# Kernel tuning notes

Hardware: AMD Instinct MI355X
Metric: run time of the kernel (lower is better)

The kernel has to match this reference:

```python
import jax, jax.numpy as jnp
import numpy as np

B, D, N, H = 4, 256, 2048, 4
HEAD_DIM = D // H


def conv1x1(W, b, x):
    # Conv1d(kernel_size=1): [B, Cin, N] -> [B, Cout, N]
    return jnp.einsum('oi,bin->bon', W, x) + b[None, :, None]


def setup_inputs() -> dict:
    key = jax.random.key(0)
    ks = jax.random.split(key, 8)
    s = 0.05
    return {
        'x': jax.random.normal(ks[0], (B, D, N), jnp.float32),
        'source': jax.random.normal(ks[1], (B, D, N), jnp.float32),
        'edge': jax.random.uniform(ks[2], (B, N, N), jnp.float32),
        'Wq': jax.random.normal(ks[3], (D, D), jnp.float32) * s,
        'bq': jnp.zeros((D,), jnp.float32),
        'Wk': jax.random.normal(ks[4], (D, D), jnp.float32) * s,
        'bk': jnp.zeros((D,), jnp.float32),
        'Wv': jax.random.normal(ks[5], (D, D), jnp.float32) * s,
        'bv': jnp.zeros((D,), jnp.float32),
        'Wm': jax.random.normal(ks[6], (D, D), jnp.float32) * s,
        'bm': jnp.zeros((D,), jnp.float32),
        'W1': jax.random.normal(ks[7], (2 * D, 2 * D), jnp.float32) * s,
        'b1': jnp.zeros((2 * D,), jnp.float32),
        'W2': jax.random.normal(jax.random.fold_in(key, 99), (D, 2 * D), jnp.float32) * s,
        'b2': jnp.zeros((D,), jnp.float32),
    }


def reference(x, source, edge, Wq, bq, Wk, bk, Wv, bv, Wm, bm, W1, b1, W2, b2):
    b = x.shape[0]
    # projections, then split channels D -> (head_dim, H), matching torch .view
    q = conv1x1(Wq, bq, x).reshape(b, HEAD_DIM, H, -1)       # [B, d, H, N]
    k = conv1x1(Wk, bk, source).reshape(b, HEAD_DIM, H, -1)  # [B, d, H, M]
    v = conv1x1(Wv, bv, source).reshape(b, HEAD_DIM, H, -1)
    scores = jnp.einsum('bdhn,bdhm->bhnm', q, k) / jnp.sqrt(jnp.float32(HEAD_DIM))
    prob = jax.nn.softmax(scores, axis=-1) * edge[:, None, :, :]  # edge-weighted probs
    msg = jnp.einsum('bhnm,bdhm->bdhn', prob, v).reshape(b, D, -1)
    message = conv1x1(Wm, bm, msg)                           # merge heads
    h = jnp.concatenate([x, message], axis=1)                # [B, 2D, N]
    h = jax.nn.relu(conv1x1(W1, b1, h))
    return conv1x1(W2, b2, h)                                # [B, D, N]
```

## Files before the change

### kernel.cpp

```cpp
#include <hip/hip_runtime.h>
#include <math.h>

#define B_ 4
#define D_ 256
#define N_ 2048
#define H_ 4

typedef __attribute__((ext_vector_type(8))) __bf16 bf16x8;
typedef __attribute__((ext_vector_type(4))) __bf16 bf16x4;
typedef __attribute__((ext_vector_type(4))) float f32x4;

template <typename OutT>
__device__ __forceinline__ void conv_tile(
    const float* __restrict__ in1, int C1,
    const float* __restrict__ in2, int C2,
    const float* __restrict__ Wt, const float* __restrict__ bias,
    OutT* __restrict__ out, int Cout, int K, int RELU, float oscale,
    int b, int o0, int n0, __bf16 (*sXT)[72])
{
    const int t = threadIdx.x;
    const int w  = t >> 6;
    const int g  = (t >> 4) & 3;
    const int c16 = t & 15;
    const int d_ld = t & 63;
    const int xcol = (t >> 6) * 16;

    f32x4 acc[4];
#pragma unroll
    for (int i = 0; i < 4; ++i) acc[i] = (f32x4){0.f, 0.f, 0.f, 0.f};

    float4 xreg[4];
    float4 wreg[4];
    const int ow = o0 + 16 * w + c16;

    auto LOADX = [&](int ks) {
        const int ch = ks + d_ld;
        const float* src = (ch < C1)
            ? in1 + ((size_t)b * C1 + ch) * N_ + n0 + xcol
            : in2 + ((size_t)b * C2 + (ch - C1)) * N_ + n0 + xcol;
#pragma unroll
        for (int j = 0; j < 4; ++j) xreg[j] = *(const float4*)&src[4 * j];
    };
    auto LOADW = [&](int ks) {
        wreg[0] = *(const float4*)&Wt[(size_t)ow * K + ks + 8 * g];
        wreg[1] = *(const float4*)&Wt[(size_t)ow * K + ks + 8 * g + 4];
        wreg[2] = *(const float4*)&Wt[(size_t)ow * K + ks + 32 + 8 * g];
        wreg[3] = *(const float4*)&Wt[(size_t)ow * K + ks + 32 + 8 * g + 4];
    };
    auto WRITEXT = [&](int buf) {
        __bf16 (*sx)[72] = sXT + (size_t)buf * 64;
#pragma unroll
        for (int j = 0; j < 4; ++j) {
            const float xf[4] = {xreg[j].x, xreg[j].y, xreg[j].z, xreg[j].w};
#pragma unroll
            for (int i = 0; i < 4; ++i)
                sx[xcol + 4 * j + i][d_ld] = (__bf16)xf[i];
        }
    };

    LOADX(0);
    LOADW(0);
    WRITEXT(0);
    __syncthreads();

    const int nsteps = K >> 6;
    for (int s = 0; s < nsteps; ++s) {
        const int cur = s & 1;
        const int ks = s << 6;
        if (s + 1 < nsteps) LOADX(ks + 64);

        bf16x8 af[2];
#pragma unroll
        for (int kc = 0; kc < 2; ++kc) {
            const float* w0 = (const float*)&wreg[2 * kc];
            const float* w1 = (const float*)&wreg[2 * kc + 1];
#pragma unroll
            for (int i = 0; i < 4; ++i) {
                af[kc][i]     = (__bf16)w0[i];
                af[kc][i + 4] = (__bf16)w1[i];
            }
        }
        if (s + 1 < nsteps) LOADW(ks + 64);

        __bf16 (*sx)[72] = sXT + (size_t)cur * 64;
#pragma unroll
        for (int kc = 0; kc < 2; ++kc)
#pragma unroll
            for (int nsub = 0; nsub < 4; ++nsub) {
                const bf16x8 bfr = *(const bf16x8*)&sx[16 * nsub + c16][32 * kc + 8 * g];
                acc[nsub] = __builtin_amdgcn_mfma_f32_16x16x32_bf16(af[kc], bfr, acc[nsub], 0, 0, 0);
            }

        if (s + 1 < nsteps) WRITEXT(cur ^ 1);
        __syncthreads();
    }

#pragma unroll
    for (int nsub = 0; nsub < 4; ++nsub)
#pragma unroll
        for (int r = 0; r < 4; ++r) {
            const int o = o0 + 16 * w + 4 * g + r;
            float v = acc[nsub][r] + bias[o];
            if (RELU) v = fmaxf(v, 0.f);
            v *= oscale;
            out[((size_t)b * Cout + o) * N_ + n0 + 16 * nsub + c16] = (OutT)v;
        }
}

template <int RELU>
__global__ __launch_bounds__(256) void mfma_conv_kernel(
    const float* __restrict__ in1, int C1,
    const float* __restrict__ in2, int C2,
    const float* __restrict__ W, const float* __restrict__ bias,
    float* __restrict__ out, int Cout, int K)
{
    __shared__ __bf16 sXT[2 * 64][72];
    conv_tile<float>(in1, C1, in2, C2, W, bias, out, Cout, K, RELU, 1.0f,
                     blockIdx.z, blockIdx.y * 64, blockIdx.x * 64, sXT);
}

__global__ __launch_bounds__(256) void qkv_conv_kernel(
    const float* __restrict__ x, const float* __restrict__ source,
    const float* __restrict__ Wq, const float* __restrict__ bq,
    const float* __restrict__ Wk, const float* __restrict__ bk,
    const float* __restrict__ Wv, const float* __restrict__ bv,
    __bf16* __restrict__ Qo, __bf16* __restrict__ Ko, __bf16* __restrict__ Vo)
{
    __shared__ __bf16 sXT[2 * 64][72];
    const int sel = blockIdx.y >> 2;
    const int o0  = (blockIdx.y & 3) * 64;
    const float* in = (sel == 0) ? x : source;
    const float* W  = (sel == 0) ? Wq : (sel == 1) ? Wk : Wv;
    const float* bs = (sel == 0) ? bq : (sel == 1) ? bk : bv;
    __bf16* out     = (sel == 0) ? Qo : (sel == 1) ? Ko : Vo;
    const float sc  = (sel == 1) ? 0.125f : 1.0f;
    conv_tile<__bf16>(in, D_, nullptr, 0, W, bs, out, D_, D_, 0, sc,
                      blockIdx.z, o0, blockIdx.x * 64, sXT);
}

template <int NSPLIT>
__global__ __launch_bounds__(256, 4) void attn_kernel(
    const __bf16* __restrict__ Qg, const __bf16* __restrict__ Kg,
    const __bf16* __restrict__ Vg, const float* __restrict__ edge,
    __bf16* __restrict__ OP, float* __restrict__ ML)
{
    const int nt    = blockIdx.x;
    const int n0    = nt * 64;
    const int split = blockIdx.y % NSPLIT;
    const int h     = blockIdx.y / NSPLIT;
    const int b     = blockIdx.z;
    const int t  = threadIdx.x;
    const int w  = t >> 6;
    const int g  = (t >> 4) & 3;
    const int c16 = t & 15;

    const int MT   = 32 / NSPLIT;
    const int m_lo = split * (N_ / NSPLIT);
    const int pid  = ((b * H_ + h) * NSPLIT + split) * 32 + nt;

    __shared__ __bf16 sKT[64][72];
    __shared__ __bf16 sP [64][72];

    bf16x8 qf[2];
#pragma unroll
    for (int kc = 0; kc < 2; ++kc)
#pragma unroll
        for (int e = 0; e < 8; ++e) {
            const int d = 32 * kc + 8 * g + e;
            qf[kc][e] = Qg[((size_t)b * D_ + d * H_ + h) * N_ + n0 + 16 * w + c16];
        }

    f32x4 acc[4];
#pragma unroll
    for (int i = 0; i < 4; ++i) acc[i] = (f32x4){0.f, 0.f, 0.f, 0.f};
    float Lr[4];
#pragma unroll
    for (int r = 0; r < 4; ++r) Lr[r] = 0.f;

    const int d_ld = t & 63;
    const int wv   = t >> 6;
    const size_t kbase = ((size_t)b * D_ + d_ld * H_ + h) * N_ + m_lo + wv * 16;
    const size_t vrow  = ((size_t)b * D_ + (16 * w + c16) * H_ + h) * N_ + m_lo;
    const size_t ebase = ((size_t)b * N_ + n0 + 16 * w + 4 * g) * N_ + m_lo + c16;

    bf16x8 kreg[2];
    bf16x8 vreg[2];
    float  ereg[4][4];

    auto LOADK = [&](int m0) {
        kreg[0] = *(const bf16x8*)&Kg[kbase + m0];
        kreg[1] = *(const bf16x8*)&Kg[kbase + m0 + 8];
    };
    auto LOADV = [&](int m0) {
        vreg[0] = *(const bf16x8*)&Vg[vrow + m0 + 8 * g];
        vreg[1] = *(const bf16x8*)&Vg[vrow + m0 + 32 + 8 * g];
    };
    auto LOADE = [&](int m0) {
#pragma unroll
        for (int r = 0; r < 4; ++r)
#pragma unroll
            for (int ms = 0; ms < 4; ++ms)
                ereg[r][ms] = edge[ebase + (size_t)r * N_ + m0 + 16 * ms];
    };
    auto WRITEKT = [&]() {
        const __bf16* kp = (const __bf16*)kreg;
#pragma unroll
        for (int i = 0; i < 16; ++i)
            sKT[wv * 16 + i][d_ld] = kp[i];
    };

    LOADK(0);
    LOADV(0);
    LOADE(0);
    WRITEKT();
    __syncthreads();

    for (int mt = 0; mt < MT; ++mt) {
        const int m0n = (mt < MT - 1 ? mt + 1 : mt) * 64;

        const bf16x8 af0 = vreg[0], af1 = vreg[1];
        LOADK(m0n);
        LOADV(m0n);

        f32x4 sfrag[4];
#pragma unroll
        for (int msub = 0; msub < 4; ++msub) {
            f32x4 s = (f32x4){0.f, 0.f, 0.f, 0.f};
#pragma unroll
            for (int kc = 0; kc < 2; ++kc) {
                const bf16x8 bfr = *(const bf16x8*)&sKT[16 * msub + c16][32 * kc + 8 * g];
                s = __builtin_amdgcn_mfma_f32_16x16x32_bf16(qf[kc], bfr, s, 0, 0, 0);
            }
            sfrag[msub] = s;
        }

#pragma unroll
        for (int msub = 0; msub < 4; ++msub) {
#pragma unroll
            for (int r = 0; r < 4; ++r) {
                const int nloc = 16 * w + 4 * g + r;
                const float p = __expf(sfrag[msub][r]);
                Lr[r] += p;
                sP[nloc][16 * msub + c16] = (__bf16)(p * ereg[r][msub]);
            }
        }
        LOADE(m0n);

        __syncthreads();

#pragma unroll
        for (int nsub = 0; nsub < 4; ++nsub) {
            const bf16x8 b0 = *(const bf16x8*)&sP[16 * nsub + c16][8 * g];
            acc[nsub] = __builtin_amdgcn_mfma_f32_16x16x32_bf16(af0, b0, acc[nsub], 0, 0, 0);
            const bf16x8 b1 = *(const bf16x8*)&sP[16 * nsub + c16][32 + 8 * g];
            acc[nsub] = __builtin_amdgcn_mfma_f32_16x16x32_bf16(af1, b1, acc[nsub], 0, 0, 0);
        }
        WRITEKT();

        __syncthreads();
    }

#pragma unroll
    for (int mask = 1; mask < 16; mask <<= 1)
#pragma unroll
        for (int r = 0; r < 4; ++r) Lr[r] += __shfl_xor(Lr[r], mask);
    if (c16 == 0) {
#pragma unroll
        for (int r = 0; r < 4; ++r) {
            const int nloc = 16 * w + 4 * g + r;
            ML[(size_t)pid * 128 + nloc]      = 0.0f;
            ML[(size_t)pid * 128 + 64 + nloc] = Lr[r];
        }
    }
#pragma unroll
    for (int nsub = 0; nsub < 4; ++nsub)
#pragma unroll
        for (int r = 0; r < 4; ++r) {
            const int dd = 16 * w + 4 * g + r;
            OP[(size_t)pid * 4096 + dd * 64 + 16 * nsub + c16] = (__bf16)acc[nsub][r];
        }
}

template <int NSPLIT>
__global__ __launch_bounds__(256) void combine_kernel(
    const __bf16* __restrict__ OP, const float* __restrict__ ML,
    float* __restrict__ msg)
{
    const int nt = blockIdx.x;
    const int h  = blockIdx.y;
    const int b  = blockIdx.z;
    const int t  = threadIdx.x;
    const int d  = t & 63;
    const int seg = t >> 6;
    const int pid0 = ((b * H_ + h) * NSPLIT) * 32 + nt;

    __shared__ float sM[NSPLIT][64], sL[NSPLIT][64];
    if (t < NSPLIT * 64) {
        const int s = t >> 6, n = t & 63;
        sM[s][n] = ML[(size_t)(pid0 + s * 32) * 128 + n];
        sL[s][n] = ML[(size_t)(pid0 + s * 32) * 128 + 64 + n];
    }
    __syncthreads();

#pragma unroll
    for (int q = 0; q < 4; ++q) {
        const int c0 = seg * 16 + q * 4;
        float o[4] = {0.f, 0.f, 0.f, 0.f};
        float wgt[NSPLIT][4];
#pragma unroll
        for (int j = 0; j < 4; ++j) {
            float mx = -3.0e38f;
            for (int s = 0; s < NSPLIT; ++s) mx = fmaxf(mx, sM[s][c0 + j]);
            float den = 0.f;
            for (int s = 0; s < NSPLIT; ++s) {
                wgt[s][j] = __expf(sM[s][c0 + j] - mx);
                den += wgt[s][j] * sL[s][c0 + j];
            }
            const float inv = 1.0f / den;
            for (int s = 0; s < NSPLIT; ++s) wgt[s][j] *= inv;
        }
        for (int s = 0; s < NSPLIT; ++s) {
            const bf16x4 a = *(const bf16x4*)&OP[(size_t)(pid0 + s * 32) * 4096 + d * 64 + c0];
#pragma unroll
            for (int j = 0; j < 4; ++j) o[j] += wgt[s][j] * (float)a[j];
        }
        float4 r = {o[0], o[1], o[2], o[3]};
        *(float4*)&msg[((size_t)b * D_ + d * H_ + h) * N_ + nt * 64 + c0] = r;
    }
}

extern "C" void kernel_launch(void* const* d_in, const int* in_sizes, int n_in,
                              void* d_out, int out_size, void* d_ws, size_t ws_size,
                              hipStream_t stream) {
    const float* x      = (const float*)d_in[0];
    const float* source = (const float*)d_in[1];
    const float* edge   = (const float*)d_in[2];
    const float* Wq = (const float*)d_in[3];
    const float* bq = (const float*)d_in[4];
    const float* Wk = (const float*)d_in[5];
    const float* bk = (const float*)d_in[6];
    const float* Wv = (const float*)d_in[7];
    const float* bv = (const float*)d_in[8];
    const float* Wm = (const float*)d_in[9];
    const float* bm = (const float*)d_in[10];
    const float* W1 = (const float*)d_in[11];
    const float* b1 = (const float*)d_in[12];
    const float* W2 = (const float*)d_in[13];
    const float* b2 = (const float*)d_in[14];
    float* out = (float*)d_out;

    const size_t BDN = (size_t)B_ * D_ * N_;
    __bf16* Qh = (__bf16*)d_ws;
    __bf16* Kh = Qh + BDN;
    __bf16* Vh = Kh + BDN;
    float*  MSG = (float*)(Vh + BDN);
    float*  MES = MSG + BDN;
    float*  H1  = MES + BDN;
    char*   tail = (char*)(H1 + 2 * BDN);
    const size_t baseBytes = (size_t)BDN * (6 + 4 + 4 + 8);

    const dim3 blk(256);
    const dim3 gD(N_ / 64, D_ / 64, B_);
    const dim3 g2D(N_ / 64, 2 * D_ / 64, B_);

    qkv_conv_kernel<<<dim3(N_ / 64, 12, B_), blk, 0, stream>>>(
        x, source, Wq, bq, Wk, bk, Wv, bv, Qh, Kh, Vh);

    auto needFor = [&](int ns) {
        const size_t pids = (size_t)ns * B_ * H_ * 32;
        return baseBytes + pids * 4096 * 2 + pids * 128 * 4;
    };
    if (ws_size >= needFor(2)) {
        const size_t pids = (size_t)2 * B_ * H_ * 32;
        __bf16* OP = (__bf16*)tail;
        float*  ML = (float*)(tail + pids * 4096 * 2);
        attn_kernel<2><<<dim3(32, H_ * 2, B_), blk, 0, stream>>>(Qh, Kh, Vh, edge, OP, ML);
        combine_kernel<2><<<dim3(32, H_, B_), blk, 0, stream>>>(OP, ML, MSG);
    } else {
        const size_t pids = (size_t)B_ * H_ * 32;
        __bf16* OP = (__bf16*)tail;
        float*  ML = (float*)(tail + pids * 4096 * 2);
        attn_kernel<1><<<dim3(32, H_, B_), blk, 0, stream>>>(Qh, Kh, Vh, edge, OP, ML);
        combine_kernel<1><<<dim3(32, H_, B_), blk, 0, stream>>>(OP, ML, MSG);
    }

    mfma_conv_kernel<0><<<gD, blk, 0, stream>>>(MSG, D_, nullptr, 0, Wm, bm, MES, D_, D_);
    mfma_conv_kernel<1><<<g2D, blk, 0, stream>>>(x, D_, MES, D_, W1, b1, H1, 2 * D_, 2 * D_);
    mfma_conv_kernel<0><<<gD, blk, 0, stream>>>(H1, 2 * D_, nullptr, 0, W2, b2, out, D_, 2 * D_);
}
```

Before: 144.1 us.

## Store intermediate activations in bf16 and double-buffer attention shared tiles

```diff
diff --git a/kernel.cpp b/kernel.cpp
--- a/kernel.cpp
+++ b/kernel.cpp
@@ -10,10 +10,25 @@
 typedef __attribute__((ext_vector_type(4))) __bf16 bf16x4;
 typedef __attribute__((ext_vector_type(4))) float f32x4;
 
-template <typename OutT>
+__device__ __forceinline__ void load_row16(const float* src, bf16x8* xs) {
+    float tmp[16];
+    *(float4*)&tmp[0]  = *(const float4*)&src[0];
+    *(float4*)&tmp[4]  = *(const float4*)&src[4];
+    *(float4*)&tmp[8]  = *(const float4*)&src[8];
+    *(float4*)&tmp[12] = *(const float4*)&src[12];
+    __bf16* o = (__bf16*)xs;
+#pragma unroll
+    for (int i = 0; i < 16; ++i) o[i] = (__bf16)tmp[i];
+}
+__device__ __forceinline__ void load_row16(const __bf16* src, bf16x8* xs) {
+    xs[0] = *(const bf16x8*)src;
+    xs[1] = *(const bf16x8*)(src + 8);
+}
+
+template <typename In1T, typename In2T, typename OutT>
 __device__ __forceinline__ void conv_tile(
-    const float* __restrict__ in1, int C1,
-    const float* __restrict__ in2, int C2,
+    const In1T* __restrict__ in1, int C1,
+    const In2T* __restrict__ in2, int C2,
     const float* __restrict__ Wt, const float* __restrict__ bias,
     OutT* __restrict__ out, int Cout, int K, int RELU, float oscale,
     int b, int o0, int n0, __bf16 (*sXT)[72])
@@ -29,17 +44,14 @@
 #pragma unroll
     for (int i = 0; i < 4; ++i) acc[i] = (f32x4){0.f, 0.f, 0.f, 0.f};
 
-    float4 xreg[4];
+    bf16x8 xs[2];
     float4 wreg[4];
     const int ow = o0 + 16 * w + c16;
 
     auto LOADX = [&](int ks) {
         const int ch = ks + d_ld;
-        const float* src = (ch < C1)
-            ? in1 + ((size_t)b * C1 + ch) * N_ + n0 + xcol
-            : in2 + ((size_t)b * C2 + (ch - C1)) * N_ + n0 + xcol;
-#pragma unroll
-        for (int j = 0; j < 4; ++j) xreg[j] = *(const float4*)&src[4 * j];
+        if (ch < C1) load_row16(in1 + ((size_t)b * C1 + ch) * N_ + n0 + xcol, xs);
+        else         load_row16(in2 + ((size_t)b * C2 + (ch - C1)) * N_ + n0 + xcol, xs);
     };
     auto LOADW = [&](int ks) {
         wreg[0] = *(const float4*)&Wt[(size_t)ow * K + ks + 8 * g];
@@ -49,13 +61,10 @@
     };
     auto WRITEXT = [&](int buf) {
         __bf16 (*sx)[72] = sXT + (size_t)buf * 64;
-#pragma unroll
-        for (int j = 0; j < 4; ++j) {
-            const float xf[4] = {xreg[j].x, xreg[j].y, xreg[j].z, xreg[j].w};
-#pragma unroll
-            for (int i = 0; i < 4; ++i)
-                sx[xcol + 4 * j + i][d_ld] = (__bf16)xf[i];
-        }
+        const __bf16* kp = (const __bf16*)xs;
+#pragma unroll
+        for (int i = 0; i < 16; ++i)
+            sx[xcol + i][d_ld] = kp[i];
     };
 
     LOADX(0);
@@ -107,16 +116,36 @@
         }
 }
 
-template <int RELU>
-__global__ __launch_bounds__(256) void mfma_conv_kernel(
+__global__ __launch_bounds__(256) void conv_hh_kernel(
+    const __bf16* __restrict__ in1, const float* __restrict__ W,
+    const float* __restrict__ bias, __bf16* __restrict__ out, int Cout, int K)
+{
+    __shared__ __bf16 sXT[2 * 64][72];
+    conv_tile<__bf16, __bf16, __bf16>(in1, K, (const __bf16*)nullptr, 0,
+        W, bias, out, Cout, K, 0, 1.0f,
+        blockIdx.z, blockIdx.y * 64, blockIdx.x * 64, sXT);
+}
+
+__global__ __launch_bounds__(256) void conv_mix_kernel(
     const float* __restrict__ in1, int C1,
-    const float* __restrict__ in2, int C2,
+    const __bf16* __restrict__ in2, int C2,
     const float* __restrict__ W, const float* __restrict__ bias,
-    float* __restrict__ out, int Cout, int K)
+    __bf16* __restrict__ out, int Cout, int K)
 {
     __shared__ __bf16 sXT[2 * 64][72];
-    conv_tile<float>(in1, C1, in2, C2, W, bias, out, Cout, K, RELU, 1.0f,
-                     blockIdx.z, blockIdx.y * 64, blockIdx.x * 64, sXT);
+    conv_tile<float, __bf16, __bf16>(in1, C1, in2, C2,
+        W, bias, out, Cout, K, 1, 1.0f,
+        blockIdx.z, blockIdx.y * 64, blockIdx.x * 64, sXT);
+}
+
+__global__ __launch_bounds__(256) void conv_hf_kernel(
+    const __bf16* __restrict__ in1, const float* __restrict__ W,
+    const float* __restrict__ bias, float* __restrict__ out, int Cout, int K)
+{
+    __shared__ __bf16 sXT[2 * 64][72];
+    conv_tile<__bf16, __bf16, float>(in1, K, (const __bf16*)nullptr, 0,
+        W, bias, out, Cout, K, 0, 1.0f,
+        blockIdx.z, blockIdx.y * 64, blockIdx.x * 64, sXT);
 }
 
 __global__ __launch_bounds__(256) void qkv_conv_kernel(
@@ -134,8 +163,9 @@
     const float* bs = (sel == 0) ? bq : (sel == 1) ? bk : bv;
     __bf16* out     = (sel == 0) ? Qo : (sel == 1) ? Ko : Vo;
     const float sc  = (sel == 1) ? 0.125f : 1.0f;
-    conv_tile<__bf16>(in, D_, nullptr, 0, W, bs, out, D_, D_, 0, sc,
-                      blockIdx.z, o0, blockIdx.x * 64, sXT);
+    conv_tile<float, float, __bf16>(in, D_, (const float*)nullptr, 0,
+        W, bs, out, D_, D_, 0, sc,
+        blockIdx.z, o0, blockIdx.x * 64, sXT);
 }
 
 template <int NSPLIT>
@@ -158,8 +188,8 @@
     const int m_lo = split * (N_ / NSPLIT);
     const int pid  = ((b * H_ + h) * NSPLIT + split) * 32 + nt;
 
-    __shared__ __bf16 sKT[64][72];
-    __shared__ __bf16 sP [64][72];
+    __shared__ __bf16 sKT[2][64][72];
+    __shared__ __bf16 sP [2][64][72];
 
     bf16x8 qf[2];
 #pragma unroll
@@ -202,20 +232,21 @@
             for (int ms = 0; ms < 4; ++ms)
                 ereg[r][ms] = edge[ebase + (size_t)r * N_ + m0 + 16 * ms];
     };
-    auto WRITEKT = [&]() {
+    auto WRITEKT = [&](int buf) {
         const __bf16* kp = (const __bf16*)kreg;
 #pragma unroll
         for (int i = 0; i < 16; ++i)
-            sKT[wv * 16 + i][d_ld] = kp[i];
+            sKT[buf][wv * 16 + i][d_ld] = kp[i];
     };
 
     LOADK(0);
     LOADV(0);
     LOADE(0);
-    WRITEKT();
+    WRITEKT(0);
     __syncthreads();
 
     for (int mt = 0; mt < MT; ++mt) {
+        const int cur = mt & 1;
         const int m0n = (mt < MT - 1 ? mt + 1 : mt) * 64;
 
         const bf16x8 af0 = vreg[0], af1 = vreg[1];
@@ -228,7 +259,7 @@
             f32x4 s = (f32x4){0.f, 0.f, 0.f, 0.f};
 #pragma unroll
             for (int kc = 0; kc < 2; ++kc) {
-                const bf16x8 bfr = *(const bf16x8*)&sKT[16 * msub + c16][32 * kc + 8 * g];
+                const bf16x8 bfr = *(const bf16x8*)&sKT[cur][16 * msub + c16][32 * kc + 8 * g];
                 s = __builtin_amdgcn_mfma_f32_16x16x32_bf16(qf[kc], bfr, s, 0, 0, 0);
             }
             sfrag[msub] = s;
@@ -241,23 +272,21 @@
                 const int nloc = 16 * w + 4 * g + r;
                 const float p = __expf(sfrag[msub][r]);
                 Lr[r] += p;
-                sP[nloc][16 * msub + c16] = (__bf16)(p * ereg[r][msub]);
+                sP[cur][nloc][16 * msub + c16] = (__bf16)(p * ereg[r][msub]);
             }
         }
         LOADE(m0n);
 
+        WRITEKT(cur ^ 1);
         __syncthreads();
 
 #pragma unroll
         for (int nsub = 0; nsub < 4; ++nsub) {
-            const bf16x8 b0 = *(const bf16x8*)&sP[16 * nsub + c16][8 * g];
+            const bf16x8 b0 = *(const bf16x8*)&sP[cur][16 * nsub + c16][8 * g];
             acc[nsub] = __builtin_amdgcn_mfma_f32_16x16x32_bf16(af0, b0, acc[nsub], 0, 0, 0);
-            const bf16x8 b1 = *(const bf16x8*)&sP[16 * nsub + c16][32 + 8 * g];
+            const bf16x8 b1 = *(const bf16x8*)&sP[cur][16 * nsub + c16][32 + 8 * g];
             acc[nsub] = __builtin_amdgcn_mfma_f32_16x16x32_bf16(af1, b1, acc[nsub], 0, 0, 0);
         }
-        WRITEKT();
-
-        __syncthreads();
     }
 
 #pragma unroll
@@ -284,7 +313,7 @@
 template <int NSPLIT>
 __global__ __launch_bounds__(256) void combine_kernel(
     const __bf16* __restrict__ OP, const float* __restrict__ ML,
-    float* __restrict__ msg)
+    __bf16* __restrict__ msg)
 {
     const int nt = blockIdx.x;
     const int h  = blockIdx.y;
@@ -324,8 +353,10 @@
 #pragma unroll
             for (int j = 0; j < 4; ++j) o[j] += wgt[s][j] * (float)a[j];
         }
-        float4 r = {o[0], o[1], o[2], o[3]};
-        *(float4*)&msg[((size_t)b * D_ + d * H_ + h) * N_ + nt * 64 + c0] = r;
+        bf16x4 r;
+#pragma unroll
+        for (int j = 0; j < 4; ++j) r[j] = (__bf16)o[j];
+        *(bf16x4*)&msg[((size_t)b * D_ + d * H_ + h) * N_ + nt * 64 + c0] = r;
     }
 }
 
@@ -350,14 +381,15 @@
     float* out = (float*)d_out;
 
     const size_t BDN = (size_t)B_ * D_ * N_;
-    __bf16* Qh = (__bf16*)d_ws;
-    __bf16* Kh = Qh + BDN;
-    __bf16* Vh = Kh + BDN;
-    float*  MSG = (float*)(Vh + BDN);
-    float*  MES = MSG + BDN;
-    float*  H1  = MES + BDN;
-    char*   tail = (char*)(H1 + 2 * BDN);
-    const size_t baseBytes = (size_t)BDN * (6 + 4 + 4 + 8);
+    char* p = (char*)d_ws;
+    __bf16* Qh  = (__bf16*)(p);
+    __bf16* Kh  = (__bf16*)(p + 2 * BDN);
+    __bf16* Vh  = (__bf16*)(p + 4 * BDN);
+    __bf16* MSG = (__bf16*)(p + 6 * BDN);
+    __bf16* MES = (__bf16*)(p + 8 * BDN);
+    __bf16* H1  = (__bf16*)(p + 10 * BDN);
+    char*   tail = p + 14 * BDN;
+    const size_t baseBytes = 14 * BDN;
 
     const dim3 blk(256);
     const dim3 gD(N_ / 64, D_ / 64, B_);
@@ -384,7 +416,7 @@
         combine_kernel<1><<<dim3(32, H_, B_), blk, 0, stream>>>(OP, ML, MSG);
     }
 
-    mfma_conv_kernel<0><<<gD, blk, 0, stream>>>(MSG, D_, nullptr, 0, Wm, bm, MES, D_, D_);
-    mfma_conv_kernel<1><<<g2D, blk, 0, stream>>>(x, D_, MES, D_, W1, b1, H1, 2 * D_, 2 * D_);
-    mfma_conv_kernel<0><<<gD, blk, 0, stream>>>(H1, 2 * D_, nullptr, 0, W2, b2, out, D_, 2 * D_);
-}
+    conv_hh_kernel<<<gD, blk, 0, stream>>>(MSG, Wm, bm, MES, D_, D_);
+    conv_mix_kernel<<<g2D, blk, 0, stream>>>(x, D_, MES, D_, W1, b1, H1, 2 * D_, 2 * D_);
+    conv_hf_kernel<<<gD, blk, 0, stream>>>(H1, W2, b2, out, D_, 2 * D_);
+}
```

New measurement: 131.9 us. 1.09x faster.
